# Optimization experiments

Measured on AMD Instinct MI355X. Metric: run time of the kernel, lower is better.

The kernel has to match this reference:

```python
import jax, jax.numpy as jnp
import numpy as np

N = 16384   # total gate nodes (64 graphs x 256 gates)
B = 64      # graphs in batch
E = 49152   # directed edges (avg in-degree 3)
Q = 32      # qubit_num
F = 256     # feat_dim
D = 2 * F   # node feature dim = 512
H = 2       # heads
A = 128     # action_num


def _gatv2(x, wl, wr, att, b, src, dst, n):
    # PyG GATv2Conv (concat=True, share_weights=False, negative_slope=0.2)
    h, c = att.shape
    xl = (x @ wl).reshape(n, h, c)   # source-side projection [N,H,C]
    xr = (x @ wr).reshape(n, h, c)   # target-side projection [N,H,C]
    e = jax.nn.leaky_relu(xl[src] + xr[dst], 0.2)       # [E,H,C]
    logit = jnp.einsum('ehc,hc->eh', e, att)             # [E,H]
    m = jax.ops.segment_max(logit, dst, num_segments=n)  # softmax over in-edges per target
    p = jnp.exp(logit - m[dst])
    den = jax.ops.segment_sum(p, dst, num_segments=n)
    alpha = p / den[dst]                                 # [E,H]
    out = jax.ops.segment_sum(alpha[:, :, None] * xl[src], dst, num_segments=n)
    return out.reshape(n, h * c) + b


def _forward(x, xt_w1, xt_b1, xt_w2, xt_b2,
             g0_wl, g0_wr, g0_att, g0_b,
             g1_wl, g1_wr, g1_att, g1_b,
             g2_wl, g2_wr, g2_att, g2_b,
             g3_wl, g3_wr, g3_att, g3_b,
             g4_wl, g4_wr, g4_att, g4_b,
             ln_w, ln_b, aggr_t,
             m_w1, m_b1, m_w2, m_b2, m_w3, m_b3,
             edge_index, batch):
    lr = lambda v: jax.nn.leaky_relu(v, 0.01)
    # x_trans: Linear -> LeakyReLU -> Linear, then fold qubit-pairs into one node
    h0 = lr(x @ xt_w1 + xt_b1) @ xt_w2 + xt_b2           # [2N, F]
    cx = h0.reshape(-1, D)                               # [N, 2F]
    n = cx.shape[0]
    # GATv2Conv default add_self_loops=True (inputs contain no self loops)
    sl = jnp.arange(n, dtype=edge_index.dtype)
    src = jnp.concatenate([edge_index[0], sl])
    dst = jnp.concatenate([edge_index[1], sl])
    res = cx
    h = lr(_gatv2(cx, g0_wl, g0_wr, g0_att, g0_b, src, dst, n))
    for wl_, wr_, att_, b_ in ((g1_wl, g1_wr, g1_att, g1_b),
                               (g2_wl, g2_wr, g2_att, g2_b),
                               (g3_wl, g3_wr, g3_att, g3_b)):
        h = lr(_gatv2(h, wl_, wr_, att_, b_, src, dst, n))
    h = lr(_gatv2(h, g4_wl, g4_wr, g4_att, g4_b, src, dst, n))
    h = h + res                                           # residual [N, 2F]
    # PyG LayerNorm(mode='graph'): normalize over nodes AND channels per graph
    cnt = jax.ops.segment_sum(jnp.ones((n,), h.dtype), batch, num_segments=B)
    norm = cnt * h.shape[1]
    mean = jax.ops.segment_sum(h.sum(-1), batch, num_segments=B) / norm
    hc = h - mean[batch][:, None]
    var = jax.ops.segment_sum((hc * hc).sum(-1), batch, num_segments=B) / norm
    h = hc / jnp.sqrt(var + 1e-5)[batch][:, None] * ln_w + ln_b
    # SoftmaxAggregation(learn=True): channel-wise softmax over nodes per graph
    logit = h * aggr_t
    mg = jax.ops.segment_max(logit, batch, num_segments=B)
    p = jnp.exp(logit - mg[batch])
    den = jax.ops.segment_sum(p, batch, num_segments=B)
    g = jax.ops.segment_sum((p / den[batch]) * h, batch, num_segments=B)  # [B, 2F]
    # head MLP 512->384->256->128
    o = lr(g @ m_w1 + m_b1)
    o = lr(o @ m_w2 + m_b2)
    return o @ m_w3 + m_b3


def setup_inputs() -> dict:
    key = jax.random.key(0)
    ks = iter(jax.random.split(key, 64))
    def rn(shp, s=0.05):
        return jax.random.normal(next(ks), shp, jnp.float32) * s
    d = {}
    d['x'] = jax.random.normal(next(ks), (2 * N, Q), jnp.float32)
    src = jax.random.randint(next(ks), (E,), 0, N, jnp.int32)
    off = jax.random.randint(next(ks), (E,), 1, N, jnp.int32)
    d['edge_index'] = jnp.stack([src, (src + off) % N])  # no self loops
    d['batch'] = jnp.arange(N, dtype=jnp.int32) // (N // B)
    d['xt_w1'] = rn((Q, F)); d['xt_b1'] = rn((F,))
    d['xt_w2'] = rn((F, F)); d['xt_b2'] = rn((F,))
    d['g0_wl'] = rn((D, H * D)); d['g0_wr'] = rn((D, H * D))
    d['g0_att'] = rn((H, D));    d['g0_b'] = rn((H * D,))
    for i in (1, 2, 3):
        d[f'g{i}_wl'] = rn((H * D, H * D)); d[f'g{i}_wr'] = rn((H * D, H * D))
        d[f'g{i}_att'] = rn((H, D));        d[f'g{i}_b'] = rn((H * D,))
    d['g4_wl'] = rn((H * D, D)); d['g4_wr'] = rn((H * D, D))
    d['g4_att'] = rn((1, D));    d['g4_b'] = rn((D,))
    d['ln_w'] = jnp.ones((D,), jnp.float32); d['ln_b'] = jnp.zeros((D,), jnp.float32)
    d['aggr_t'] = jnp.array(1.0, jnp.float32)
    d['m_w1'] = rn((D, 384)); d['m_b1'] = rn((384,))
    d['m_w2'] = rn((384, 256)); d['m_b2'] = rn((256,))
    d['m_w3'] = rn((256, A)); d['m_b3'] = rn((A,))
    return d


def reference(x, edge_index, batch, xt_w1, xt_b1, xt_w2, xt_b2,
              g0_wl, g0_wr, g0_att, g0_b,
              g1_wl, g1_wr, g1_att, g1_b,
              g2_wl, g2_wr, g2_att, g2_b,
              g3_wl, g3_wr, g3_att, g3_b,
              g4_wl, g4_wr, g4_att, g4_b,
              ln_w, ln_b, aggr_t,
              m_w1, m_b1, m_w2, m_b2, m_w3, m_b3):
    return _forward(x, xt_w1, xt_b1, xt_w2, xt_b2,
                    g0_wl, g0_wr, g0_att, g0_b,
                    g1_wl, g1_wr, g1_att, g1_b,
                    g2_wl, g2_wr, g2_att, g2_b,
                    g3_wl, g3_wr, g3_att, g3_b,
                    g4_wl, g4_wr, g4_att, g4_b,
                    ln_w, ln_b, aggr_t,
                    m_w1, m_b1, m_w2, m_b2, m_w3, m_b3,
                    edge_index, batch)
```

## Files before the change

kernel.cpp:

```cpp
#include <hip/hip_runtime.h>
#include <hip/hip_bf16.h>

typedef __hip_bfloat16 bf16;

#define NN 16384
#define BBG 64
#define EE 49152
#define ET (EE + NN)
#define DD 512
#define NG (NN / BBG)

__device__ __forceinline__ float b2f(bf16 v) { return __bfloat162float(v); }
__device__ __forceinline__ bf16 f2b(float v) { return __float2bfloat16(v); }
__device__ __forceinline__ float sb2f(short s) {
    unsigned u = ((unsigned)(unsigned short)s) << 16;
    return __builtin_bit_cast(float, u);
}
__device__ __forceinline__ short f2bs(float v) {
    bf16 b = f2b(v);
    return __builtin_bit_cast(short, b);
}
__device__ __forceinline__ int clampi(int v, int lo, int hi)
{
    return v < lo ? lo : (v > hi ? hi : v);
}

typedef __attribute__((ext_vector_type(8))) short bf16x8;
typedef __attribute__((ext_vector_type(4))) float f32x4;

#define AS1 __attribute__((address_space(1)))
#define AS3 __attribute__((address_space(3)))

__global__ __launch_bounds__(256) void gemm_mfma_bt(
    const bf16* __restrict__ A, const bf16* __restrict__ Bt,
    const float* __restrict__ bias, float* __restrict__ C,
    bf16* __restrict__ Cb, int M, int N, int K, float slope, int has_act)
{
    __shared__ bf16 As[128 * 32];
    __shared__ bf16 Bs[128 * 32];
    const int tid = threadIdx.x;
    const int w = tid >> 6;
    const int l = tid & 63;
    const int bm = blockIdx.y * 128;
    const int bn = blockIdx.x * 128;
    const int wrow = (w >> 1) * 64;
    const int wcol = (w & 1) * 64;
    const int quad = l >> 4;
    const int c16 = l & 15;

    const int lrow = l >> 2;
    const int lchunk = l & 3;
    const bf16* Ag = A + (size_t)(bm + w * 16 + lrow) * K + lchunk * 8;
    const bf16* Bg = Bt + (size_t)(bn + w * 16 + lrow) * K + lchunk * 8;
    char* AsB = (char*)As;
    char* BsB = (char*)Bs;

    f32x4 acc[4][4] = {};

    for (int k0 = 0; k0 < K; k0 += 32) {
        __builtin_amdgcn_global_load_lds((const AS1 void*)(Ag + k0),
            (AS3 void*)(AsB + w * 1024), 16, 0, 0);
        __builtin_amdgcn_global_load_lds((const AS1 void*)(Ag + (size_t)64 * K + k0),
            (AS3 void*)(AsB + 4096 + w * 1024), 16, 0, 0);
        __builtin_amdgcn_global_load_lds((const AS1 void*)(Bg + k0),
            (AS3 void*)(BsB + w * 1024), 16, 0, 0);
        __builtin_amdgcn_global_load_lds((const AS1 void*)(Bg + (size_t)64 * K + k0),
            (AS3 void*)(BsB + 4096 + w * 1024), 16, 0, 0);
        __syncthreads();

        bf16x8 a[4], b[4];
#pragma unroll
        for (int i = 0; i < 4; i++) {
            int ra = wrow + i * 16 + c16;
            a[i] = *(const bf16x8*)(AsB + ra * 64 + quad * 16);
            int rb = wcol + i * 16 + c16;
            b[i] = *(const bf16x8*)(BsB + rb * 64 + quad * 16);
        }
#pragma unroll
        for (int i = 0; i < 4; i++)
#pragma unroll
            for (int j = 0; j < 4; j++)
                acc[i][j] = __builtin_amdgcn_mfma_f32_16x16x32_bf16(
                    a[i], b[j], acc[i][j], 0, 0, 0);
        __syncthreads();
    }

#pragma unroll
    for (int i = 0; i < 4; i++) {
#pragma unroll
        for (int j = 0; j < 4; j++) {
            int col = bn + wcol + j * 16 + c16;
            float bv = bias ? bias[col] : 0.f;
#pragma unroll
            for (int r = 0; r < 4; r++) {
                int row = bm + wrow + i * 16 + quad * 4 + r;
                float v = acc[i][j][r] + bv;
                if (has_act) v = (v >= 0.f) ? v : v * slope;
                if (C)  C[(size_t)row * N + col] = v;
                if (Cb) Cb[(size_t)row * N + col] = f2b(v);
            }
        }
    }
}

__global__ __launch_bounds__(256) void gemm_f32(
    const float* __restrict__ A, const float* __restrict__ W,
    const float* __restrict__ bias, float* __restrict__ C,
    int M, int N, int K, float slope, int has_act)
{
    const int BK = 16;
    __shared__ float Asm[BK][64 + 1];
    __shared__ float Wsm[BK][64 + 1];
    int tid = threadIdx.x;
    int bm = blockIdx.y * 64;
    int bn = blockIdx.x * 64;
    int tr = tid >> 4;
    int tc = tid & 15;
    float acc[4][4] = {};

    for (int k0 = 0; k0 < K; k0 += BK) {
        {
            int col = tid & 15;
            int row = tid >> 4;
#pragma unroll
            for (int p = 0; p < 4; p++) {
                int r = row + p * 16;
                Asm[col][r] = A[(size_t)(bm + r) * K + k0 + col];
            }
        }
        {
            int wc = tid & 63;
            int wr = tid >> 6;
#pragma unroll
            for (int p = 0; p < 4; p++) {
                int r = wr + p * 4;
                Wsm[r][wc] = W[(size_t)(k0 + r) * N + bn + wc];
            }
        }
        __syncthreads();
#pragma unroll
        for (int kk = 0; kk < BK; kk++) {
            float a[4], w[4];
#pragma unroll
            for (int i = 0; i < 4; i++) a[i] = Asm[kk][tr * 4 + i];
#pragma unroll
            for (int j = 0; j < 4; j++) w[j] = Wsm[kk][tc * 4 + j];
#pragma unroll
            for (int i = 0; i < 4; i++)
#pragma unroll
                for (int j = 0; j < 4; j++)
                    acc[i][j] += a[i] * w[j];
        }
        __syncthreads();
    }
#pragma unroll
    for (int i = 0; i < 4; i++) {
        int r = bm + tr * 4 + i;
#pragma unroll
        for (int j = 0; j < 4; j++) {
            int cn = bn + tc * 4 + j;
            float v = acc[i][j];
            if (bias) v += bias[cn];
            if (has_act) v = (v >= 0.f) ? v : v * slope;
            C[(size_t)r * N + cn] = v;
        }
    }
}

__global__ __launch_bounds__(256) void transpose_f2b2(
    const float* __restrict__ in0, bf16* __restrict__ out0,
    const float* __restrict__ in1, bf16* __restrict__ out1, int R, int C)
{
    const float* in = blockIdx.z ? in1 : in0;
    bf16* out = blockIdx.z ? out1 : out0;
    __shared__ float tile[32][33];
    int c0 = blockIdx.x * 32;
    int r0 = blockIdx.y * 32;
    int tx = threadIdx.x & 31;
    int ty = threadIdx.x >> 5;
#pragma unroll
    for (int k = 0; k < 4; k++) {
        int r = ty + k * 8;
        tile[r][tx] = in[(size_t)(r0 + r) * C + c0 + tx];
    }
    __syncthreads();
#pragma unroll
    for (int k = 0; k < 4; k++) {
        int rr = ty + k * 8;
        out[(size_t)(c0 + rr) * R + r0 + tx] = f2b(tile[tx][rr]);
    }
}

__global__ void f2b_vec(const float* __restrict__ in, bf16* __restrict__ out, int n)
{
    int i = blockIdx.x * 256 + threadIdx.x;
    if (i < n) out[i] = f2b(in[i]);
}

__global__ void count_deg(const int* __restrict__ ei, int* __restrict__ deg)
{
    int e = blockIdx.x * 256 + threadIdx.x;
    if (e >= ET) return;
    int d = (e < EE) ? ei[EE + e] : (e - EE);
    d = clampi(d, 0, NN - 1);
    atomicAdd(&deg[d], 1);
}

__global__ __launch_bounds__(256) void scan_deg(const int* __restrict__ deg,
                                                int* __restrict__ rs)
{
    __shared__ int part[256];
    __shared__ int psum[257];
    int tid = threadIdx.x;
    const int per = NN / 256;
    int base = tid * per;
    int s = 0;
    for (int i = 0; i < per; i++) s += deg[base + i];
    part[tid] = s;
    __syncthreads();
    if (tid == 0) {
        int acc = 0;
        for (int i = 0; i < 256; i++) { psum[i] = acc; acc += part[i]; }
        psum[256] = acc;
    }
    __syncthreads();
    int acc = psum[tid];
    for (int i = 0; i < per; i++) { rs[base + i] = acc; acc += deg[base + i]; }
    if (tid == 0) rs[NN] = psum[256];
}

__global__ void fill_csr(const int* __restrict__ ei, const int* __restrict__ rs,
                         int* __restrict__ cur, int* __restrict__ csrc)
{
    int e = blockIdx.x * 256 + threadIdx.x;
    if (e >= ET) return;
    int s, d;
    if (e < EE) { s = ei[e]; d = ei[EE + e]; } else { s = d = e - EE; }
    s = clampi(s, 0, NN - 1);
    d = clampi(d, 0, NN - 1);
    int pos = atomicAdd(&cur[d], 1);
    int slot = clampi(rs[d] + pos, 0, ET - 1);
    csrc[slot] = s;
}

template<int HC>
__global__ __launch_bounds__(256) void gat_wave(
    const bf16* __restrict__ xl, const bf16* __restrict__ xr,
    const float* __restrict__ att, const float* __restrict__ bias,
    const int* __restrict__ rs, const int* __restrict__ csrc,
    const float* __restrict__ res, float* __restrict__ out_f,
    bf16* __restrict__ out_b, float* __restrict__ lnsums)
{
    constexpr int CPL = HC / 64;
    constexpr int NV = CPL / 8;
    const int tid = threadIdx.x;
    const int w = tid >> 6;
    const int lane = tid & 63;
    const int n = blockIdx.x * 4 + w;
    const int c0 = lane * CPL;

    int start = rs[n];
    int deg = clampi(rs[n + 1] - start, 1, 64);
    start = clampi(start, 0, ET - 1);
    int my_src = 0;
    if (lane < deg) my_src = clampi(csrc[start + lane], 0, NN - 1);

    float av[CPL], rv[CPL];
    {
        bf16x8 rp[NV];
#pragma unroll
        for (int v = 0; v < NV; v++)
            rp[v] = *(const bf16x8*)(xr + (size_t)n * HC + c0 + v * 8);
#pragma unroll
        for (int k = 0; k < CPL; k++) {
            rv[k] = sb2f(rp[k / 8][k % 8]);
            av[k] = att[c0 + k];
        }
    }

    float m = -1e30f, den = 0.f;
    float acc[CPL];
#pragma unroll
    for (int k = 0; k < CPL; k++) acc[k] = 0.f;

    auto loadrow = [&](int i, bf16x8* dst) {
        int s = __shfl(my_src, i);
        const bf16* rp = xl + (size_t)s * HC + c0;
#pragma unroll
        for (int v = 0; v < NV; v++) dst[v] = *(const bf16x8*)(rp + v * 8);
    };

    bf16x8 cur[NV], nx1[NV], nx2[NV];
    loadrow(0, cur);
    if (deg > 1) loadrow(1, nx1);
    if (deg > 2) loadrow(2, nx2);

    for (int i = 0; i < deg; i++) {
        bf16x8 nxt[NV];
        if (i + 3 < deg) loadrow(i + 3, nxt);

        float part = 0.f;
#pragma unroll
        for (int k = 0; k < CPL; k++) {
            float x = sb2f(cur[k / 8][k % 8]);
            float u = x + rv[k];
            u = (u >= 0.f) ? u : 0.2f * u;
            part = fmaf(av[k], u, part);
        }
        if (HC == 1024) {
#pragma unroll
            for (int msk = 16; msk; msk >>= 1) part += __shfl_xor(part, msk);
        } else {
#pragma unroll
            for (int msk = 32; msk; msk >>= 1) part += __shfl_xor(part, msk);
        }
        float lg = part;

        float mn = fmaxf(m, lg);
        float r = __expf(m - mn);
        float pi = __expf(lg - mn);
        m = mn;
        den = den * r + pi;
#pragma unroll
        for (int k = 0; k < CPL; k++) {
            float x = sb2f(cur[k / 8][k % 8]);
            acc[k] = fmaf(acc[k], r, pi * x);
        }
#pragma unroll
        for (int v = 0; v < NV; v++) { cur[v] = nx1[v]; nx1[v] = nx2[v]; nx2[v] = nxt[v]; }
    }

    float inv = 1.f / den;
    float ls = 0.f, ls2 = 0.f;
    float vals[CPL];
#pragma unroll
    for (int k = 0; k < CPL; k++) {
        float v = fmaf(acc[k], inv, bias[c0 + k]);
        v = (v >= 0.f) ? v : 0.01f * v;
        vals[k] = v;
    }
    if (res) {
#pragma unroll
        for (int k = 0; k < CPL; k++) {
            vals[k] += res[(size_t)n * HC + c0 + k];
            ls += vals[k];
            ls2 += vals[k] * vals[k];
        }
#pragma unroll
        for (int v = 0; v < NV * 2; v++) {
            f32x4 ov;
#pragma unroll
            for (int k = 0; k < 4; k++) ov[k] = vals[v * 4 + k];
            *(f32x4*)(out_f + (size_t)n * HC + c0 + v * 4) = ov;
        }
    } else {
#pragma unroll
        for (int v = 0; v < NV; v++) {
            bf16x8 ov;
#pragma unroll
            for (int k = 0; k < 8; k++) ov[k] = f2bs(vals[v * 8 + k]);
            *(bf16x8*)(out_b + (size_t)n * HC + c0 + v * 8) = ov;
        }
    }

    if (lnsums) {
#pragma unroll
        for (int msk = 32; msk; msk >>= 1) {
            ls += __shfl_xor(ls, msk);
            ls2 += __shfl_xor(ls2, msk);
        }
        if (lane == 0) {
            int g = n >> 8;
            atomicAdd(&lnsums[g], ls);
            atomicAdd(&lnsums[BBG + g], ls2);
        }
    }
}

__global__ __launch_bounds__(256) void aggr_partial(
    const float* __restrict__ h, const float* __restrict__ lnsums,
    const float* __restrict__ lnw, const float* __restrict__ lnb,
    const float* __restrict__ t_, float* __restrict__ pm,
    float* __restrict__ pd, float* __restrict__ pa)
{
    int g = blockIdx.x, ch = blockIdx.y, nk = blockIdx.z;
    int tid = threadIdx.x;
    int c = ch * 256 + tid;
    const float tot = (float)(NG * DD);
    float S = lnsums[g], S2 = lnsums[BBG + g];
    float mu = S / tot;
    float iv = rsqrtf(fmaxf(S2 / tot - mu * mu, 0.f) + 1e-5f);
    float w = lnw[c], b = lnb[c], t = t_[0];
    size_t base = (size_t)g * NG * DD + (size_t)nk * 64 * DD + c;
    float m = -1e30f, den = 0.f, acc = 0.f;
    for (int i = 0; i < 64; i++) {
        float hn = (h[base + (size_t)i * DD] - mu) * iv * w + b;
        float lg = hn * t;
        if (lg > m) {
            float r = __expf(m - lg);
            den *= r; acc *= r; m = lg;
        }
        float p = __expf(lg - m);
        den += p; acc += p * hn;
    }
    size_t idx = (((size_t)g * 2 + ch) * 4 + nk) * 256 + tid;
    pm[idx] = m; pd[idx] = den; pa[idx] = acc;
}

__global__ __launch_bounds__(256) void aggr_combine(
    const float* __restrict__ pm, const float* __restrict__ pd,
    const float* __restrict__ pa, float* __restrict__ gout)
{
    int g = blockIdx.x, ch = blockIdx.y;
    int tid = threadIdx.x;
    size_t base = (((size_t)g * 2 + ch) * 4) * 256 + tid;
    float m = -1e30f;
#pragma unroll
    for (int k = 0; k < 4; k++) m = fmaxf(m, pm[base + k * 256]);
    float den = 0.f, acc = 0.f;
#pragma unroll
    for (int k = 0; k < 4; k++) {
        float r = __expf(pm[base + k * 256] - m);
        den += pd[base + k * 256] * r;
        acc += pa[base + k * 256] * r;
    }
    gout[(size_t)g * DD + ch * 256 + tid] = acc / den;
}

extern "C" void kernel_launch(void* const* d_in, const int* in_sizes, int n_in,
                              void* d_out, int out_size, void* d_ws, size_t ws_size,
                              hipStream_t stream)
{
    const float* x      = (const float*)d_in[0];
    const int*   ei     = (const int*)d_in[1];
    const float* xt_w1  = (const float*)d_in[3];
    const float* xt_b1  = (const float*)d_in[4];
    const float* xt_w2  = (const float*)d_in[5];
    const float* xt_b2  = (const float*)d_in[6];
    const float* ln_w   = (const float*)d_in[27];
    const float* ln_b   = (const float*)d_in[28];
    const float* aggr_t = (const float*)d_in[29];
    const float* m_w1   = (const float*)d_in[30];
    const float* m_b1   = (const float*)d_in[31];
    const float* m_w2   = (const float*)d_in[32];
    const float* m_b2   = (const float*)d_in[33];
    const float* m_w3   = (const float*)d_in[34];
    const float* m_b3   = (const float*)d_in[35];
    float* out = (float*)d_out;

    char* p = (char*)d_ws;
    auto take = [&](size_t bytes) {
        char* r = p;
        p += (bytes + 255) & ~(size_t)255;
        return r;
    };
    int* i_deg     = (int*)take((size_t)(NN + 1) * 4);
    int* i_rs      = (int*)take((size_t)(NN + 1) * 4);
    int* i_cur     = (int*)take((size_t)NN * 4);
    int* i_src     = (int*)take((size_t)ET * 4);
    float* f_sums  = (float*)take((size_t)2 * BBG * 4);
    float* f_pm    = (float*)take((size_t)BBG * 2 * 4 * 256 * 4);
    float* f_pd    = (float*)take((size_t)BBG * 2 * 4 * 256 * 4);
    float* f_pa    = (float*)take((size_t)BBG * 2 * 4 * 256 * 4);
    float* b_g     = (float*)take((size_t)BBG * DD * 4);
    float* b_m1    = (float*)take((size_t)BBG * 384 * 4);
    float* b_m2    = (float*)take((size_t)BBG * 256 * 4);
    float* b_res   = (float*)take((size_t)NN * DD * 4);
    float* b_h     = (float*)take((size_t)NN * DD * 4);
    bf16* b_resb   = (bf16*)take((size_t)NN * DD * 2);
    bf16* b_hb     = (bf16*)take((size_t)NN * 1024 * 2);
    bf16* b_xlb    = (bf16*)take((size_t)NN * 1024 * 2);
    bf16* b_xrb    = (bf16*)take((size_t)NN * 1024 * 2);
    bf16* b_xb     = (bf16*)take((size_t)2 * NN * 32 * 2);
    bf16* b_wlb    = (bf16*)take((size_t)1024 * 1024 * 2);
    bf16* b_wrb    = (bf16*)take((size_t)1024 * 1024 * 2);
    bf16* b_w1b    = (bf16*)take((size_t)32 * 256 * 2);
    bf16* b_w2b    = (bf16*)take((size_t)256 * 256 * 2);
    bf16* b_t1b = b_hb;

    dim3 blk(256);

    hipMemsetAsync(i_deg, 0, (size_t)(NN + 1) * 4, stream);
    hipMemsetAsync(i_cur, 0, (size_t)NN * 4, stream);
    hipMemsetAsync(f_sums, 0, (size_t)2 * BBG * 4, stream);
    count_deg<<<ET / 256, blk, 0, stream>>>(ei, i_deg);
    scan_deg<<<1, blk, 0, stream>>>(i_deg, i_rs);
    fill_csr<<<ET / 256, blk, 0, stream>>>(ei, i_rs, i_cur, i_src);

    f2b_vec<<<(2 * NN * 32 + 255) / 256, blk, 0, stream>>>(x, b_xb, 2 * NN * 32);
    transpose_f2b2<<<dim3(256 / 32, 32 / 32, 1), blk, 0, stream>>>(
        xt_w1, b_w1b, xt_w1, b_w1b, 32, 256);
    transpose_f2b2<<<dim3(256 / 32, 256 / 32, 1), blk, 0, stream>>>(
        xt_w2, b_w2b, xt_w2, b_w2b, 256, 256);

    gemm_mfma_bt<<<dim3(256 / 128, 32768 / 128), blk, 0, stream>>>(
        b_xb, b_w1b, xt_b1, (float*)nullptr, b_t1b, 32768, 256, 32, 0.01f, 1);
    gemm_mfma_bt<<<dim3(256 / 128, 32768 / 128), blk, 0, stream>>>(
        b_t1b, b_w2b, xt_b2, b_res, b_resb, 32768, 256, 256, 0.f, 0);

    for (int L = 0; L < 5; L++) {
        const float* wl  = (const float*)d_in[7 + 4 * L];
        const float* wr  = (const float*)d_in[8 + 4 * L];
        const float* att = (const float*)d_in[9 + 4 * L];
        const float* gb  = (const float*)d_in[10 + 4 * L];
        int Fin = (L == 0) ? 512 : 1024;
        int HC  = (L == 4) ? 512 : 1024;
        const bf16* hin = (L == 0) ? b_resb : b_hb;

        transpose_f2b2<<<dim3(HC / 32, Fin / 32, 2), blk, 0, stream>>>(
            wl, b_wlb, wr, b_wrb, Fin, HC);
        gemm_mfma_bt<<<dim3(HC / 128, NN / 128), blk, 0, stream>>>(
            hin, b_wlb, (const float*)nullptr, (float*)nullptr, b_xlb,
            NN, HC, Fin, 0.f, 0);
        gemm_mfma_bt<<<dim3(HC / 128, NN / 128), blk, 0, stream>>>(
            hin, b_wrb, (const float*)nullptr, (float*)nullptr, b_xrb,
            NN, HC, Fin, 0.f, 0);
        if (L == 4) {
            gat_wave<512><<<NN / 4, blk, 0, stream>>>(
                b_xlb, b_xrb, att, gb, i_rs, i_src,
                b_res, b_h, (bf16*)nullptr, f_sums);
        } else {
            gat_wave<1024><<<NN / 4, blk, 0, stream>>>(
                b_xlb, b_xrb, att, gb, i_rs, i_src,
                (const float*)nullptr, (float*)nullptr, b_hb, (float*)nullptr);
        }
    }

    aggr_partial<<<dim3(BBG, 2, 4), blk, 0, stream>>>(
        b_h, f_sums, ln_w, ln_b, aggr_t, f_pm, f_pd, f_pa);
    aggr_combine<<<dim3(BBG, 2), blk, 0, stream>>>(f_pm, f_pd, f_pa, b_g);

    gemm_f32<<<dim3(384 / 64, 1), blk, 0, stream>>>(
        b_g, m_w1, m_b1, b_m1, 64, 384, 512, 0.01f, 1);
    gemm_f32<<<dim3(256 / 64, 1), blk, 0, stream>>>(
        b_m1, m_w2, m_b2, b_m2, 64, 256, 384, 0.01f, 1);
    gemm_f32<<<dim3(128 / 64, 1), blk, 0, stream>>>(
        b_m2, m_w3, m_b3, out, 64, 128, 256, 0.f, 0);
}
```

Measured before the change: 1.162 ms.

## Fuse left/right GAT projections into one GEMM and deepen gather prefetch

The two per-layer projection GEMMs (x@wl, x@wr) become a single GEMM over concatenated transposed weights, and each output column is routed to xl or xr. This halves the number of passes over the input activations and cuts launches. The GAT gather kernel now preloads up to six neighbour rows up front with an occupancy hint, in place of a rolling three-deep pipeline. The attention-aggregation partial split goes from four to eight chunks for more parallelism. The deeper prefetch raises register pressure, which could limit occupancy.

Result: faster. 1.041 ms (-10.4%).

```diff
diff --git a/kernel.cpp b/kernel.cpp
--- a/kernel.cpp
+++ b/kernel.cpp
@@ -98,6 +98,75 @@
                 if (has_act) v = (v >= 0.f) ? v : v * slope;
                 if (C)  C[(size_t)row * N + col] = v;
                 if (Cb) Cb[(size_t)row * N + col] = f2b(v);
+            }
+        }
+    }
+}
+
+__global__ __launch_bounds__(256) void gemm_mfma_dual(
+    const bf16* __restrict__ A, const bf16* __restrict__ Bt,
+    bf16* __restrict__ X0, bf16* __restrict__ X1,
+    int M, int Ntot, int K, int HC)
+{
+    __shared__ bf16 As[128 * 32];
+    __shared__ bf16 Bs[128 * 32];
+    const int tid = threadIdx.x;
+    const int w = tid >> 6;
+    const int l = tid & 63;
+    const int bm = blockIdx.y * 128;
+    const int bn = blockIdx.x * 128;
+    const int wrow = (w >> 1) * 64;
+    const int wcol = (w & 1) * 64;
+    const int quad = l >> 4;
+    const int c16 = l & 15;
+
+    const int lrow = l >> 2;
+    const int lchunk = l & 3;
+    const bf16* Ag = A + (size_t)(bm + w * 16 + lrow) * K + lchunk * 8;
+    const bf16* Bg = Bt + (size_t)(bn + w * 16 + lrow) * K + lchunk * 8;
+    char* AsB = (char*)As;
+    char* BsB = (char*)Bs;
+
+    f32x4 acc[4][4] = {};
+
+    for (int k0 = 0; k0 < K; k0 += 32) {
+        __builtin_amdgcn_global_load_lds((const AS1 void*)(Ag + k0),
+            (AS3 void*)(AsB + w * 1024), 16, 0, 0);
+        __builtin_amdgcn_global_load_lds((const AS1 void*)(Ag + (size_t)64 * K + k0),
+            (AS3 void*)(AsB + 4096 + w * 1024), 16, 0, 0);
+        __builtin_amdgcn_global_load_lds((const AS1 void*)(Bg + k0),
+            (AS3 void*)(BsB + w * 1024), 16, 0, 0);
+        __builtin_amdgcn_global_load_lds((const AS1 void*)(Bg + (size_t)64 * K + k0),
+            (AS3 void*)(BsB + 4096 + w * 1024), 16, 0, 0);
+        __syncthreads();
+
+        bf16x8 a[4], b[4];
+#pragma unroll
+        for (int i = 0; i < 4; i++) {
+            int ra = wrow + i * 16 + c16;
+            a[i] = *(const bf16x8*)(AsB + ra * 64 + quad * 16);
+            int rb = wcol + i * 16 + c16;
+            b[i] = *(const bf16x8*)(BsB + rb * 64 + quad * 16);
+        }
+#pragma unroll
+        for (int i = 0; i < 4; i++)
+#pragma unroll
+            for (int j = 0; j < 4; j++)
+                acc[i][j] = __builtin_amdgcn_mfma_f32_16x16x32_bf16(
+                    a[i], b[j], acc[i][j], 0, 0, 0);
+        __syncthreads();
+    }
+
+#pragma unroll
+    for (int i = 0; i < 4; i++) {
+#pragma unroll
+        for (int j = 0; j < 4; j++) {
+            int col = bn + wcol + j * 16 + c16;
+            bf16* dst = (col < HC) ? (X0 + col) : (X1 + col - HC);
+#pragma unroll
+            for (int r = 0; r < 4; r++) {
+                int row = bm + wrow + i * 16 + quad * 4 + r;
+                dst[(size_t)row * HC] = f2b(acc[i][j][r]);
             }
         }
     }
@@ -244,7 +313,7 @@
 }
 
 template<int HC>
-__global__ __launch_bounds__(256) void gat_wave(
+__global__ __launch_bounds__(256, 4) void gat_wave2(
     const bf16* __restrict__ xl, const bf16* __restrict__ xr,
     const float* __restrict__ att, const float* __restrict__ bias,
     const int* __restrict__ rs, const int* __restrict__ csrc,
@@ -253,6 +322,7 @@
 {
     constexpr int CPL = HC / 64;
     constexpr int NV = CPL / 8;
+    constexpr int PF = 6;
     const int tid = threadIdx.x;
     const int w = tid >> 6;
     const int lane = tid & 63;
@@ -278,31 +348,27 @@
         }
     }
 
+    bf16x8 rows[PF][NV];
+#pragma unroll
+    for (int r = 0; r < PF; r++) {
+        if (r < deg) {
+            int s = __shfl(my_src, r);
+            const bf16* rp = xl + (size_t)s * HC + c0;
+#pragma unroll
+            for (int v = 0; v < NV; v++) rows[r][v] = *(const bf16x8*)(rp + v * 8);
+        }
+    }
+
     float m = -1e30f, den = 0.f;
     float acc[CPL];
 #pragma unroll
     for (int k = 0; k < CPL; k++) acc[k] = 0.f;
 
-    auto loadrow = [&](int i, bf16x8* dst) {
-        int s = __shfl(my_src, i);
-        const bf16* rp = xl + (size_t)s * HC + c0;
-#pragma unroll
-        for (int v = 0; v < NV; v++) dst[v] = *(const bf16x8*)(rp + v * 8);
-    };
-
-    bf16x8 cur[NV], nx1[NV], nx2[NV];
-    loadrow(0, cur);
-    if (deg > 1) loadrow(1, nx1);
-    if (deg > 2) loadrow(2, nx2);
-
-    for (int i = 0; i < deg; i++) {
-        bf16x8 nxt[NV];
-        if (i + 3 < deg) loadrow(i + 3, nxt);
-
+    auto process = [&](bf16x8 (&rw)[NV]) {
         float part = 0.f;
 #pragma unroll
         for (int k = 0; k < CPL; k++) {
-            float x = sb2f(cur[k / 8][k % 8]);
+            float x = sb2f(rw[k / 8][k % 8]);
             float u = x + rv[k];
             u = (u >= 0.f) ? u : 0.2f * u;
             part = fmaf(av[k], u, part);
@@ -315,7 +381,6 @@
             for (int msk = 32; msk; msk >>= 1) part += __shfl_xor(part, msk);
         }
         float lg = part;
-
         float mn = fmaxf(m, lg);
         float r = __expf(m - mn);
         float pi = __expf(lg - mn);
@@ -323,11 +388,34 @@
         den = den * r + pi;
 #pragma unroll
         for (int k = 0; k < CPL; k++) {
-            float x = sb2f(cur[k / 8][k % 8]);
+            float x = sb2f(rw[k / 8][k % 8]);
             acc[k] = fmaf(acc[k], r, pi * x);
         }
-#pragma unroll
-        for (int v = 0; v < NV; v++) { cur[v] = nx1[v]; nx1[v] = nx2[v]; nx2[v] = nxt[v]; }
+    };
+
+#pragma unroll
+    for (int i = 0; i < PF; i++)
+        if (i < deg) process(rows[i]);
+
+    if (deg > PF) {
+        bf16x8 curv[NV], nxt[NV];
+        {
+            int s = __shfl(my_src, PF);
+            const bf16* rp = xl + (size_t)s * HC + c0;
+#pragma unroll
+            for (int v = 0; v < NV; v++) curv[v] = *(const bf16x8*)(rp + v * 8);
+        }
+        for (int i = PF; i < deg; i++) {
+            if (i + 1 < deg) {
+                int s = __shfl(my_src, i + 1);
+                const bf16* rp = xl + (size_t)s * HC + c0;
+#pragma unroll
+                for (int v = 0; v < NV; v++) nxt[v] = *(const bf16x8*)(rp + v * 8);
+            }
+            process(curv);
+#pragma unroll
+            for (int v = 0; v < NV; v++) curv[v] = nxt[v];
+        }
     }
 
     float inv = 1.f / den;
@@ -391,9 +479,9 @@
     float mu = S / tot;
     float iv = rsqrtf(fmaxf(S2 / tot - mu * mu, 0.f) + 1e-5f);
     float w = lnw[c], b = lnb[c], t = t_[0];
-    size_t base = (size_t)g * NG * DD + (size_t)nk * 64 * DD + c;
+    size_t base = (size_t)g * NG * DD + (size_t)nk * 32 * DD + c;
     float m = -1e30f, den = 0.f, acc = 0.f;
-    for (int i = 0; i < 64; i++) {
+    for (int i = 0; i < 32; i++) {
         float hn = (h[base + (size_t)i * DD] - mu) * iv * w + b;
         float lg = hn * t;
         if (lg > m) {
@@ -403,7 +491,7 @@
         float p = __expf(lg - m);
         den += p; acc += p * hn;
     }
-    size_t idx = (((size_t)g * 2 + ch) * 4 + nk) * 256 + tid;
+    size_t idx = (((size_t)g * 2 + ch) * 8 + nk) * 256 + tid;
     pm[idx] = m; pd[idx] = den; pa[idx] = acc;
 }
 
@@ -413,13 +501,13 @@
 {
     int g = blockIdx.x, ch = blockIdx.y;
     int tid = threadIdx.x;
-    size_t base = (((size_t)g * 2 + ch) * 4) * 256 + tid;
+    size_t base = (((size_t)g * 2 + ch) * 8) * 256 + tid;
     float m = -1e30f;
 #pragma unroll
-    for (int k = 0; k < 4; k++) m = fmaxf(m, pm[base + k * 256]);
+    for (int k = 0; k < 8; k++) m = fmaxf(m, pm[base + k * 256]);
     float den = 0.f, acc = 0.f;
 #pragma unroll
-    for (int k = 0; k < 4; k++) {
+    for (int k = 0; k < 8; k++) {
         float r = __expf(pm[base + k * 256] - m);
         den += pd[base + k * 256] * r;
         acc += pa[base + k * 256] * r;
@@ -459,9 +547,9 @@
     int* i_cur     = (int*)take((size_t)NN * 4);
     int* i_src     = (int*)take((size_t)ET * 4);
     float* f_sums  = (float*)take((size_t)2 * BBG * 4);
-    float* f_pm    = (float*)take((size_t)BBG * 2 * 4 * 256 * 4);
-    float* f_pd    = (float*)take((size_t)BBG * 2 * 4 * 256 * 4);
-    float* f_pa    = (float*)take((size_t)BBG * 2 * 4 * 256 * 4);
+    float* f_pm    = (float*)take((size_t)BBG * 2 * 8 * 256 * 4);
+    float* f_pd    = (float*)take((size_t)BBG * 2 * 8 * 256 * 4);
+    float* f_pa    = (float*)take((size_t)BBG * 2 * 8 * 256 * 4);
     float* b_g     = (float*)take((size_t)BBG * DD * 4);
     float* b_m1    = (float*)take((size_t)BBG * 384 * 4);
     float* b_m2    = (float*)take((size_t)BBG * 256 * 4);
@@ -472,8 +560,7 @@
     bf16* b_xlb    = (bf16*)take((size_t)NN * 1024 * 2);
     bf16* b_xrb    = (bf16*)take((size_t)NN * 1024 * 2);
     bf16* b_xb     = (bf16*)take((size_t)2 * NN * 32 * 2);
-    bf16* b_wlb    = (bf16*)take((size_t)1024 * 1024 * 2);
-    bf16* b_wrb    = (bf16*)take((size_t)1024 * 1024 * 2);
+    bf16* b_wcat   = (bf16*)take((size_t)2048 * 1024 * 2);
     bf16* b_w1b    = (bf16*)take((size_t)32 * 256 * 2);
     bf16* b_w2b    = (bf16*)take((size_t)256 * 256 * 2);
     bf16* b_t1b = b_hb;
@@ -508,25 +595,21 @@
         const bf16* hin = (L == 0) ? b_resb : b_hb;
 
         transpose_f2b2<<<dim3(HC / 32, Fin / 32, 2), blk, 0, stream>>>(
-            wl, b_wlb, wr, b_wrb, Fin, HC);
-        gemm_mfma_bt<<<dim3(HC / 128, NN / 128), blk, 0, stream>>>(
-            hin, b_wlb, (const float*)nullptr, (float*)nullptr, b_xlb,
-            NN, HC, Fin, 0.f, 0);
-        gemm_mfma_bt<<<dim3(HC / 128, NN / 128), blk, 0, stream>>>(
-            hin, b_wrb, (const float*)nullptr, (float*)nullptr, b_xrb,
-            NN, HC, Fin, 0.f, 0);
+            wl, b_wcat, wr, b_wcat + (size_t)HC * Fin, Fin, HC);
+        gemm_mfma_dual<<<dim3(2 * HC / 128, NN / 128), blk, 0, stream>>>(
+            hin, b_wcat, b_xlb, b_xrb, NN, 2 * HC, Fin, HC);
         if (L == 4) {
-            gat_wave<512><<<NN / 4, blk, 0, stream>>>(
+            gat_wave2<512><<<NN / 4, blk, 0, stream>>>(
                 b_xlb, b_xrb, att, gb, i_rs, i_src,
                 b_res, b_h, (bf16*)nullptr, f_sums);
         } else {
-            gat_wave<1024><<<NN / 4, blk, 0, stream>>>(
+            gat_wave2<1024><<<NN / 4, blk, 0, stream>>>(
                 b_xlb, b_xrb, att, gb, i_rs, i_src,
                 (const float*)nullptr, (float*)nullptr, b_hb, (float*)nullptr);
         }
     }
 
-    aggr_partial<<<dim3(BBG, 2, 4), blk, 0, stream>>>(
+    aggr_partial<<<dim3(BBG, 2, 8), blk, 0, stream>>>(
         b_h, f_sums, ln_w, ln_b, aggr_t, f_pm, f_pd, f_pa);
     aggr_combine<<<dim3(BBG, 2), blk, 0, stream>>>(f_pm, f_pd, f_pa, b_g);
 
```
